# Performance work log

Hardware: AMD Instinct MI355X
Metric: run time of the kernel (lower is better)

Reference implementation:

```python
import jax, jax.numpy as jnp
import numpy as np

B, SC, ST = 16, 512, 512
DP, DC = 256, 128
D = DP + 2 * DC          # 512 = d_model
H, L, DFF = 8, 2, 2048
NCAT, NCONT = 1000, 2048


def sin_embed(vals, d, scale=1000.0):
    # vectorized sinusoidal_time_embedding: even dims -> sin(angle), odd dims -> cos(angle)
    i = jnp.arange(d, dtype=jnp.float32)
    ang = vals.astype(jnp.float32)[..., None] / jnp.power(scale, i / d)
    return jnp.where(i % 2 == 0, jnp.sin(ang), jnp.cos(ang))


def layer_norm(x, g, b, eps=1e-5):
    m = jnp.mean(x, -1, keepdims=True)
    v = jnp.mean(jnp.square(x - m), -1, keepdims=True)
    return (x - m) / jnp.sqrt(v + eps) * g + b


def setup_inputs() -> dict:
    key = jax.random.key(0)
    ks = jax.random.split(key, 16)
    s = 0.02
    def n(k, shape, scale=s):
        return jax.random.normal(k, shape, dtype=jnp.float32) * scale
    return {
        "context_cat": jax.random.randint(ks[0], (B, SC), 0, NCAT),
        "context_time": jax.random.uniform(ks[1], (B, SC), dtype=jnp.float32) * 100.0,
        "context_f0": jax.random.uniform(ks[2], (B, SC), dtype=jnp.float32) * 500.0,
        "target_cat": jax.random.randint(ks[3], (B, ST), 0, NCAT),
        "target_time": jax.random.uniform(ks[4], (B, ST), dtype=jnp.float32) * 100.0,
        "target_f0": jax.random.uniform(ks[5], (B, ST), dtype=jnp.float32) * 500.0,
        "cat_table": n(ks[6], (NCAT, DP), 1.0),
        "cont_table": sin_embed(jnp.arange(NCONT, dtype=jnp.float32), DC),  # frozen sin table
        "pad_emb": n(ks[7], (D,), 1.0),
        "Wq": n(ks[8], (L, D, D)), "bq": jnp.zeros((L, D)),
        "Wk": n(ks[9], (L, D, D)), "bk": jnp.zeros((L, D)),
        "Wv": n(ks[10], (L, D, D)), "bv": jnp.zeros((L, D)),
        "Wo": n(ks[11], (L, D, D)), "bo": jnp.zeros((L, D)),
        "ln1g": jnp.ones((L, D)), "ln1b": jnp.zeros((L, D)),
        "ln2g": jnp.ones((L, D)), "ln2b": jnp.zeros((L, D)),
        "W1": n(ks[12], (L, D, DFF)), "b1": jnp.zeros((L, DFF)),
        "W2": n(ks[13], (L, DFF, D)), "b2": jnp.zeros((L, D)),
    }


def reference(context_cat, context_time, context_f0, target_cat, target_time, target_f0,
              cat_table, cont_table, pad_emb,
              Wq, bq, Wk, bk, Wv, bv, Wo, bo,
              ln1g, ln1b, ln2g, ln2b, W1, b1, W2, b2):
    def embed(cat, tm, f0):
        pad = cat < 0
        e = jnp.concatenate(
            [cat_table[jnp.maximum(cat, 0)], sin_embed(tm, DC), sin_embed(f0, DC)], axis=-1)
        return jnp.where(pad[..., None], pad_emb, e), pad

    ce, cp = embed(context_cat, context_time, context_f0)
    te, tp = embed(target_cat, target_time, target_f0)
    x = jnp.concatenate([ce, te], axis=1)                       # [B, SC+ST, D]
    bias = jnp.where(jnp.concatenate([cp, tp], 1), -1e9, 0.0)[:, None, None, :]
    hd = D // H
    inv_sqrt = 1.0 / np.sqrt(hd).astype(np.float32)

    def step(h, p):
        wq, bq_, wk, bk_, wv, bv_, wo, bo_, g1, c1, g2, c2, w1, d1, w2, d2 = p
        Bn, S, _ = h.shape
        q = (h @ wq + bq_).reshape(Bn, S, H, hd)
        k = (h @ wk + bk_).reshape(Bn, S, H, hd)
        v = (h @ wv + bv_).reshape(Bn, S, H, hd)
        scores = jnp.einsum('bqhd,bkhd->bhqk', q, k) * inv_sqrt + bias
        attn = jax.nn.softmax(scores, axis=-1)
        o = jnp.einsum('bhqk,bkhd->bqhd', attn, v).reshape(Bn, S, D)
        h = layer_norm(h + o @ wo + bo_, g1, c1)                # post-norm (torch default)
        f = jax.nn.relu(h @ w1 + d1) @ w2 + d2
        return layer_norm(h + f, g2, c2), None

    x, _ = jax.lax.scan(step, x, (Wq, bq, Wk, bk, Wv, bv, Wo, bo,
                                  ln1g, ln1b, ln2g, ln2b, W1, b1, W2, b2))
    out = x[:, SC:, :]
    pred_cat = out[..., :DP] @ cat_table.T
    pred_time = out[..., DP:DP + DC] @ cont_table.T
    pred_f0 = out[..., DP + DC:] @ cont_table.T
    return pred_cat, pred_time, pred_f0
```

## Files before the change

### kernel.cpp

```cpp
#include <hip/hip_runtime.h>


typedef _Float16 half8 __attribute__((ext_vector_type(8)));
typedef _Float16 half4 __attribute__((ext_vector_type(4)));
typedef float f32x4 __attribute__((ext_vector_type(4)));

__device__ __forceinline__ void gl2lds16(const _Float16* g, _Float16* l) {
    __builtin_amdgcn_global_load_lds(
        (const __attribute__((address_space(1))) void*)g,
        (__attribute__((address_space(3))) void*)l, 16, 0, 0);
}

__global__ void cast_f32_f16_k(const float* __restrict__ in, _Float16* __restrict__ out,
                               long nsrc, long ntot) {
    long i = (long)blockIdx.x * blockDim.x + threadIdx.x;
    long stride = (long)gridDim.x * blockDim.x;
    for (; i < ntot; i += stride) out[i] = i < nsrc ? (_Float16)in[i] : (_Float16)0.f;
}

__global__ void tcast_k(const float* __restrict__ in, _Float16* __restrict__ out,
                        int R, int C, long zs, int rowoff) {
    __shared__ float tile[32][33];
    long z = blockIdx.z;
    const float* src = in + z * (long)R * C;
    _Float16* dst = out + z * zs + (long)rowoff * R;
    int c0 = blockIdx.x * 32, r0 = blockIdx.y * 32;
    for (int i = threadIdx.y; i < 32; i += 8)
        tile[i][threadIdx.x] = src[(long)(r0 + i) * C + c0 + threadIdx.x];
    __syncthreads();
    for (int i = threadIdx.y; i < 32; i += 8)
        dst[(long)(c0 + i) * R + r0 + threadIdx.x] = (_Float16)tile[threadIdx.x][i];
}

__global__ void bcat_k(const float* __restrict__ bq, const float* __restrict__ bk,
                       const float* __restrict__ bv, float* __restrict__ out, int L) {
    int i = blockIdx.x * 256 + threadIdx.x;
    if (i >= L * 1536) return;
    int l = i / 1536, j = i - l * 1536;
    float v = j < 512 ? bq[l * 512 + j] : (j < 1024 ? bk[l * 512 + j - 512] : bv[l * 512 + j - 1024]);
    out[i] = v;
}

__global__ void vtrans_k(const _Float16* __restrict__ qkv, _Float16* __restrict__ vT) {
    __shared__ _Float16 tile[32][33];
    int bh = blockIdx.z; int b = bh >> 3, h = bh & 7;
    int s0 = blockIdx.x * 32, d0 = blockIdx.y * 32;
    const _Float16* src = qkv + ((long)b * 1024) * 1536 + 1024 + h * 64;
    _Float16* dst = vT + (long)bh * 64 * 1024;
    for (int i = threadIdx.y; i < 32; i += 8)
        tile[i][threadIdx.x] = src[(long)(s0 + i) * 1536 + d0 + threadIdx.x];
    __syncthreads();
    for (int i = threadIdx.y; i < 32; i += 8)
        dst[(long)(d0 + i) * 1024 + s0 + threadIdx.x] = tile[threadIdx.x][i];
}

__global__ __launch_bounds__(128) void embed_k(
    const int* __restrict__ ccat, const float* __restrict__ ctime, const float* __restrict__ cf0,
    const int* __restrict__ tcat, const float* __restrict__ ttime, const float* __restrict__ tf0,
    const float* __restrict__ cat_table, const float* __restrict__ pad_emb,
    float* __restrict__ xf, _Float16* __restrict__ xb, float* __restrict__ biasKey) {
    int t = blockIdx.x;
    int b = t >> 10, s = t & 1023;
    int j = b * 512 + (s & 511);
    int cat; float tm, f0;
    if (s < 512) { cat = ccat[j]; tm = ctime[j]; f0 = cf0[j]; }
    else         { cat = tcat[j]; tm = ttime[j]; f0 = tf0[j]; }
    bool pad = cat < 0;
    if (threadIdx.x == 0) biasKey[t] = pad ? -1e9f : 0.f;
    int c = cat < 0 ? 0 : cat;
    #pragma unroll
    for (int u = 0; u < 4; u++) {
        int d = threadIdx.x * 4 + u;
        float val;
        if (pad) val = pad_emb[d];
        else if (d < 256) val = cat_table[(long)c * 256 + d];
        else {
            float base = (d < 384) ? tm : f0;
            int i = (d < 384) ? (d - 256) : (d - 384);
            float ang = base / powf(1000.f, (float)i * (1.f / 128.f));
            val = (i & 1) ? cosf(ang) : sinf(ang);
        }
        long o = (long)t * 512 + d;
        xf[o] = val;
        xb[o] = (_Float16)val;
    }
}

__global__ __launch_bounds__(256) void layernorm_k(
    float* xf, _Float16* __restrict__ xb,
    const float* __restrict__ g, const float* __restrict__ beta) {
    long row = blockIdx.x;
    int tid = threadIdx.x;
    float* xr = xf + row * 512;
    float v0 = xr[tid], v1 = xr[tid + 256];
    float s = v0 + v1, q = v0 * v0 + v1 * v1;
    #pragma unroll
    for (int o = 32; o; o >>= 1) { s += __shfl_down(s, o); q += __shfl_down(q, o); }
    __shared__ float rs[4], rq[4];
    if ((tid & 63) == 0) { rs[tid >> 6] = s; rq[tid >> 6] = q; }
    __syncthreads();
    s = rs[0] + rs[1] + rs[2] + rs[3];
    q = rq[0] + rq[1] + rq[2] + rq[3];
    float mean = s * (1.f / 512.f);
    float var = q * (1.f / 512.f) - mean * mean;
    float rstd = rsqrtf(var + 1e-5f);
    float y0 = (v0 - mean) * rstd * g[tid] + beta[tid];
    float y1 = (v1 - mean) * rstd * g[tid + 256] + beta[tid + 256];
    xr[tid] = y0; xr[tid + 256] = y1;
    xb[row * 512 + tid] = (_Float16)y0;
    xb[row * 512 + tid + 256] = (_Float16)y1;
}

__global__ __launch_bounds__(256, 3) void flash_k(
    const _Float16* __restrict__ QKV, const _Float16* __restrict__ VT,
    const float* __restrict__ biasKey, _Float16* __restrict__ O) {
    const int S = 1024, D = 512, LDQ = 1536, NT = 16;
    int bh = blockIdx.x; int b = bh >> 3, h = bh & 7;
    int qt = blockIdx.y;
    int tid = threadIdx.x, w = tid >> 6, lane = tid & 63;
    int g = lane >> 4, q15 = lane & 15;

    __shared__ __align__(16) _Float16 Ks[2][64 * 64];
    __shared__ __align__(16) _Float16 VTs[2][64 * 64];
    __shared__ __align__(16) _Float16 Ps[4][16][72];
    __shared__ __align__(16) float biasLds[1024];

    {
        const float* bsrc = biasKey + (long)b * S;
        f32x4 bv4 = *(const f32x4*)&bsrc[tid * 4];
        #pragma unroll
        for (int r = 0; r < 4; r++) bv4[r] *= 1.442695041f;
        *(f32x4*)&biasLds[tid * 4] = bv4;
    }

    int qrow = qt * 64 + w * 16 + q15;
    const _Float16* qp = QKV + ((long)(b * S + qrow)) * LDQ + h * 64 + g * 8;
    half8 qf[2];
    qf[0] = *(const half8*)(qp);
    qf[1] = *(const half8*)(qp + 32);
    const _Float16 qsc = (_Float16)0.1803368801f;
    #pragma unroll
    for (int kk = 0; kk < 2; kk++)
        #pragma unroll
        for (int i = 0; i < 8; i++) qf[kk][i] *= qsc;

    const _Float16* kbase = QKV + 512 + ((long)b * S) * LDQ + h * 64;
    const _Float16* vbase = VT + (long)bh * 64 * S;

    auto stageK = [&](int buf, int kt) {
        #pragma unroll
        for (int i = 0; i < 2; i++) {
            int c = tid + i * 256;
            int row = c >> 3, p = c & 7;
            int s = p ^ (row & 7);
            gl2lds16(kbase + (long)(kt * 64 + row) * LDQ + s * 8, &Ks[buf][c * 8]);
        }
    };
    auto stageV = [&](int buf, int kt) {
        #pragma unroll
        for (int i = 0; i < 2; i++) {
            int c = tid + i * 256;
            int row = c >> 3, p = c & 7;
            int s = p ^ (row & 7);
            gl2lds16(vbase + (long)row * S + kt * 64 + s * 8, &VTs[buf][c * 8]);
        }
    };

    f32x4 acc_o[4];
    #pragma unroll
    for (int i = 0; i < 4; i++)
        #pragma unroll
        for (int r = 0; r < 4; r++) acc_o[i][r] = 0.f;
    float m_run = -1e30f, l_run = 0.f;

    auto QK = [&](int kt, f32x4 (&s)[4]) {
        #pragma unroll
        for (int mf = 0; mf < 4; mf++)
            #pragma unroll
            for (int r = 0; r < 4; r++) s[mf][r] = 0.f;
        int buf = kt & 1;
        __builtin_amdgcn_s_setprio(1);
        #pragma unroll
        for (int kk = 0; kk < 2; kk++)
            #pragma unroll
            for (int mf = 0; mf < 4; mf++) {
                int row = mf * 16 + q15;
                half8 kf = *(const half8*)&Ks[buf][row * 64 + (((kk * 4 + g) ^ (row & 7)) * 8)];
                s[mf] = __builtin_amdgcn_mfma_f32_16x16x32_f16(kf, qf[kk], s[mf], 0, 0, 0);
            }
        __builtin_amdgcn_s_setprio(0);
    };

    auto SMPV = [&](int kt, f32x4 (&s)[4]) {
        float mt = -1e30f;
        #pragma unroll
        for (int mf = 0; mf < 4; mf++) {
            f32x4 b4 = *(const f32x4*)&biasLds[kt * 64 + mf * 16 + g * 4];
            #pragma unroll
            for (int r = 0; r < 4; r++) {
                float sv = s[mf][r] + b4[r];
                s[mf][r] = sv;
                mt = fmaxf(mt, sv);
            }
        }
        mt = fmaxf(mt, __shfl_xor(mt, 16));
        mt = fmaxf(mt, __shfl_xor(mt, 32));

        float rsum = 0.f;
        if (__all(mt - m_run <= 8.f)) {
            #pragma unroll
            for (int mf = 0; mf < 4; mf++)
                #pragma unroll
                for (int r = 0; r < 4; r++) {
                    float p = exp2f(s[mf][r] - m_run);
                    s[mf][r] = p; rsum += p;
                }
        } else {
            float m_new = fmaxf(m_run, mt);
            float scale = exp2f(m_run - m_new);
            #pragma unroll
            for (int mf = 0; mf < 4; mf++)
                #pragma unroll
                for (int r = 0; r < 4; r++) {
                    float p = exp2f(s[mf][r] - m_new);
                    s[mf][r] = p; rsum += p;
                }
            float sc[4];
            #pragma unroll
            for (int r = 0; r < 4; r++) sc[r] = __shfl(scale, g * 4 + r);
            #pragma unroll
            for (int nf = 0; nf < 4; nf++)
                #pragma unroll
                for (int r = 0; r < 4; r++) acc_o[nf][r] *= sc[r];
            l_run *= scale;
            m_run = m_new;
        }
        rsum += __shfl_xor(rsum, 16);
        rsum += __shfl_xor(rsum, 32);
        l_run += rsum;

        #pragma unroll
        for (int mf = 0; mf < 4; mf++) {
            half4 h4;
            #pragma unroll
            for (int r = 0; r < 4; r++) h4[r] = (_Float16)s[mf][r];
            *(half4*)&Ps[w][q15][mf * 16 + g * 4] = h4;
        }

        int buf = kt & 1;
        __builtin_amdgcn_s_setprio(1);
        #pragma unroll
        for (int kk = 0; kk < 2; kk++) {
            half8 pa = *(const half8*)&Ps[w][q15][kk * 32 + g * 8];
            #pragma unroll
            for (int nf = 0; nf < 4; nf++) {
                int row = nf * 16 + q15;
                half8 vf = *(const half8*)&VTs[buf][row * 64 + (((kk * 4 + g) ^ (row & 7)) * 8)];
                acc_o[nf] = __builtin_amdgcn_mfma_f32_16x16x32_f16(pa, vf, acc_o[nf], 0, 0, 0);
            }
        }
        __builtin_amdgcn_s_setprio(0);
    };

    f32x4 sA[4], sB[4];
    stageK(0, 0); stageV(0, 0); stageK(1, 1);
    __syncthreads();
    QK(0, sA);

    for (int t = 0; t < NT; t += 2) {
        __syncthreads();
        if (t + 2 < NT) stageK(t & 1, t + 2);
        if (t + 1 < NT) stageV((t + 1) & 1, t + 1);
        if (t + 1 < NT) QK(t + 1, sB);
        SMPV(t, sA);
        __syncthreads();
        if (t + 3 < NT) stageK((t + 1) & 1, t + 3);
        if (t + 2 < NT) stageV(t & 1, t + 2);
        if (t + 2 < NT) QK(t + 2, sA);
        SMPV(t + 1, sB);
    }

    float linv = 1.f / l_run;
    float lv[4];
    #pragma unroll
    for (int r = 0; r < 4; r++) lv[r] = __shfl(linv, g * 4 + r);
    _Float16* obase = O + ((long)(b * S + qt * 64 + w * 16)) * D + h * 64;
    #pragma unroll
    for (int nf = 0; nf < 4; nf++)
        #pragma unroll
        for (int r = 0; r < 4; r++) {
            int row = g * 4 + r;
            obase[(long)row * D + nf * 16 + q15] = (_Float16)(acc_o[nf][r] * lv[r]);
        }
}

__global__ __launch_bounds__(256) void gemm_nt(
    const _Float16* __restrict__ A, long lda, long sA1, long sA2,
    const _Float16* __restrict__ Bm, long ldb, long sB1, long sB2,
    float* Cf, _Float16* Cb, long ldc, long sC1, long sC2,
    const float* __restrict__ bias, long sb1, long sb2,
    const float* resid,
    int M, int N, int K, int Z2, float alpha, int relu) {
    int z = blockIdx.z;
    int z1 = z / Z2, z2 = z - z1 * Z2;
    A  += z1 * sA1 + z2 * sA2;
    Bm += z1 * sB1 + z2 * sB2;
    long coff = z1 * sC1 + z2 * sC2;
    if (bias) bias += z1 * sb1 + z2 * sb2;

    int gx = gridDim.x;
    int nwg = gx * gridDim.y;
    int bid = blockIdx.y * gx + blockIdx.x;
    int q = nwg >> 3, r = nwg & 7;
    int xcd = bid & 7, ii = bid >> 3;
    int swz = (xcd < r ? xcd * (q + 1) : r * (q + 1) + (xcd - r) * q) + ii;
    int m0 = (swz / gx) * 128;
    int n0 = (swz % gx) * 128;

    __shared__ __align__(16) _Float16 As[3][128 * 32];
    __shared__ __align__(16) _Float16 Bs[3][128 * 32];

    int tid = threadIdx.x;
    int lane = tid & 63;
    int w = tid >> 6;
    int wr = (w >> 1) << 6;
    int wc = (w & 1) << 6;

    f32x4 acc[4][4];
    #pragma unroll
    for (int i = 0; i < 4; i++)
        #pragma unroll
        for (int jj = 0; jj < 4; jj++) { acc[i][jj][0] = 0.f; acc[i][jj][1] = 0.f; acc[i][jj][2] = 0.f; acc[i][jj][3] = 0.f; }

    int fr = lane & 15;
    int g = lane >> 4;
    int rs8 = (g ^ (fr & 3)) * 8;

    auto stage = [&](int buf, int kt) {
        #pragma unroll
        for (int i = 0; i < 2; i++) {
            int idx = tid + i * 256;
            int row = idx >> 2, s = idx & 3;
            int sg = s ^ (row & 3);
            gl2lds16(A + (long)(m0 + row) * lda + kt * 32 + sg * 8, &As[buf][idx * 8]);
            gl2lds16(Bm + (long)(n0 + row) * ldb + kt * 32 + sg * 8, &Bs[buf][idx * 8]);
        }
    };

    int nk = K >> 5;
    stage(0, 0);
    stage(1, 1);

    for (int t = 0; t < nk; ++t) {
        if (t + 1 < nk) asm volatile("s_waitcnt vmcnt(4)" ::: "memory");
        else            asm volatile("s_waitcnt vmcnt(0)" ::: "memory");
        __builtin_amdgcn_s_barrier();
        __builtin_amdgcn_sched_barrier(0);
        int cur = t % 3;
        if (t + 2 < nk) stage((t + 2) % 3, t + 2);

        half8 af[4], bfv[4];
        #pragma unroll
        for (int m = 0; m < 4; m++) af[m] = *(const half8*)&As[cur][(wr + m * 16 + fr) * 32 + rs8];
        #pragma unroll
        for (int n = 0; n < 4; n++) bfv[n] = *(const half8*)&Bs[cur][(wc + n * 16 + fr) * 32 + rs8];
        #pragma unroll
        for (int m = 0; m < 4; m++)
            #pragma unroll
            for (int n = 0; n < 4; n++)
                acc[m][n] = __builtin_amdgcn_mfma_f32_16x16x32_f16(af[m], bfv[n], acc[m][n], 0, 0, 0);
    }

    int fq = lane >> 4;
    #pragma unroll
    for (int m = 0; m < 4; m++) {
        #pragma unroll
        for (int jj = 0; jj < 4; jj++) {
            long row = m0 + wr + m * 16 + fq * 4 + jj;
            #pragma unroll
            for (int n = 0; n < 4; n++) {
                int col = n0 + wc + n * 16 + fr;
                if (col < N) {
                    float v = acc[m][n][jj] * alpha;
                    if (bias) v += bias[col];
                    long o = coff + row * ldc + col;
                    if (resid) v += resid[o];
                    if (relu) v = fmaxf(v, 0.f);
                    if (Cf) Cf[o] = v;
                    if (Cb) Cb[o] = (_Float16)v;
                }
            }
        }
    }
}

extern "C" void kernel_launch(void* const* d_in, const int* in_sizes, int n_in,
                              void* d_out, int out_size, void* d_ws, size_t ws_size,
                              hipStream_t stream) {
    const int Bn = 16, S = 1024, D = 512, H = 8, L = 2, DFF = 2048, NCAT = 1000, NCONT = 2048;
    const long M = (long)Bn * S;

    const int*   ccat      = (const int*)d_in[0];
    const float* ctime     = (const float*)d_in[1];
    const float* cf0       = (const float*)d_in[2];
    const int*   tcat      = (const int*)d_in[3];
    const float* ttime     = (const float*)d_in[4];
    const float* tf0       = (const float*)d_in[5];
    const float* cat_table = (const float*)d_in[6];
    const float* cont_tab  = (const float*)d_in[7];
    const float* pad_emb   = (const float*)d_in[8];
    const float* Wq = (const float*)d_in[9];
    const float* bq = (const float*)d_in[10];
    const float* Wk = (const float*)d_in[11];
    const float* bk = (const float*)d_in[12];
    const float* Wv = (const float*)d_in[13];
    const float* bv = (const float*)d_in[14];
    const float* Wo = (const float*)d_in[15];
    const float* bo = (const float*)d_in[16];
    const float* ln1g = (const float*)d_in[17];
    const float* ln1b = (const float*)d_in[18];
    const float* ln2g = (const float*)d_in[19];
    const float* ln2b = (const float*)d_in[20];
    const float* W1 = (const float*)d_in[21];
    const float* b1 = (const float*)d_in[22];
    const float* W2 = (const float*)d_in[23];
    const float* b2 = (const float*)d_in[24];

    char* wsb = (char*)d_ws;
    size_t off = 0;
    auto alloc = [&](size_t bytes) -> void* {
        off = (off + 255) & ~(size_t)255;
        void* p = wsb + off; off += bytes; return p;
    };

    float*     xf      = (float*)alloc(M * D * 4);
    _Float16*  xb      = (_Float16*)alloc(M * D * 2);
    _Float16*  qkv     = (_Float16*)alloc(M * 3 * D * 2);
    _Float16*  vT      = (_Float16*)alloc(M * D * 2);
    _Float16*  ob      = (_Float16*)alloc(M * D * 2);
    float*     biasKey = (float*)alloc(M * 4);
    _Float16*  WqkvT = (_Float16*)alloc((size_t)L * 3 * D * D * 2);
    float*     bqkv  = (float*)alloc((size_t)L * 3 * D * 4);
    _Float16*  WoT  = (_Float16*)alloc((size_t)L * D * D * 2);
    _Float16*  W1T  = (_Float16*)alloc((size_t)L * D * DFF * 2);
    _Float16*  W2T  = (_Float16*)alloc((size_t)L * DFF * D * 2);
    _Float16*  catT = (_Float16*)alloc((size_t)1024 * 256 * 2);
    _Float16*  conT = (_Float16*)alloc((size_t)NCONT * 128 * 2);

    size_t need_ffh = (size_t)M * DFF * 2;
    _Float16* ffh;
    size_t offAl = (off + 255) & ~(size_t)255;
    if (offAl + need_ffh <= ws_size) ffh = (_Float16*)alloc(need_ffh);
    else ffh = (_Float16*)d_out;

    auto gemm = [&](const _Float16* A, long lda, long sA1, long sA2,
                    const _Float16* Bm, long ldb, long sB1, long sB2,
                    float* Cf, _Float16* Cb, long ldc, long sC1, long sC2,
                    const float* bias, long sb1, long sb2,
                    const float* resid, int Mm, int Nn, int Kk,
                    int Z1, int Z2, float alpha, int relu) {
        dim3 gdim((Nn + 127) / 128, (Mm + 127) / 128, Z1 * Z2);
        gemm_nt<<<gdim, 256, 0, stream>>>(A, lda, sA1, sA2, Bm, ldb, sB1, sB2,
                                          Cf, Cb, ldc, sC1, sC2, bias, sb1, sb2,
                                          resid, Mm, Nn, Kk, Z2, alpha, relu);
    };

    dim3 tb(32, 8);
    tcast_k<<<dim3(D / 32, D / 32, L), tb, 0, stream>>>(Wq, WqkvT, D, D, (long)3 * D * D, 0);
    tcast_k<<<dim3(D / 32, D / 32, L), tb, 0, stream>>>(Wk, WqkvT, D, D, (long)3 * D * D, D);
    tcast_k<<<dim3(D / 32, D / 32, L), tb, 0, stream>>>(Wv, WqkvT, D, D, (long)3 * D * D, 2 * D);
    bcat_k<<<dim3((L * 1536 + 255) / 256), 256, 0, stream>>>(bq, bk, bv, bqkv, L);
    tcast_k<<<dim3(D / 32, D / 32, L), tb, 0, stream>>>(Wo, WoT, D, D, (long)D * D, 0);
    tcast_k<<<dim3(DFF / 32, D / 32, L), tb, 0, stream>>>(W1, W1T, D, DFF, (long)D * DFF, 0);
    tcast_k<<<dim3(D / 32, DFF / 32, L), tb, 0, stream>>>(W2, W2T, DFF, D, (long)DFF * D, 0);
    cast_f32_f16_k<<<dim3(512), 256, 0, stream>>>(cat_table, catT, (long)NCAT * 256, (long)1024 * 256);
    cast_f32_f16_k<<<dim3(512), 256, 0, stream>>>(cont_tab, conT, (long)NCONT * 128, (long)NCONT * 128);

    embed_k<<<dim3((unsigned)M), 128, 0, stream>>>(ccat, ctime, cf0, tcat, ttime, tf0,
                                                   cat_table, pad_emb, xf, xb, biasKey);

    for (int l = 0; l < L; l++) {
        gemm(xb, D, 0, 0, WqkvT + (size_t)l * 3 * D * D, D, 0, 0, nullptr, qkv, 3 * D, 0, 0,
             bqkv + (size_t)l * 3 * D, 0, 0, nullptr, (int)M, 3 * D, D, 1, 1, 1.f, 0);
        vtrans_k<<<dim3(32, 2, Bn * H), tb, 0, stream>>>(qkv, vT);

        flash_k<<<dim3(Bn * H, S / 64), 256, 0, stream>>>(qkv, vT, biasKey, ob);

        gemm(ob, D, 0, 0, WoT + (size_t)l * D * D, D, 0, 0, xf, nullptr, D, 0, 0,
             bo + l * D, 0, 0, xf, (int)M, D, D, 1, 1, 1.f, 0);
        layernorm_k<<<dim3((unsigned)M), 256, 0, stream>>>(xf, xb, ln1g + l * D, ln1b + l * D);

        gemm(xb, D, 0, 0, W1T + (size_t)l * D * DFF, D, 0, 0, nullptr, ffh, DFF, 0, 0,
             b1 + l * DFF, 0, 0, nullptr, (int)M, DFF, D, 1, 1, 1.f, 1);
        gemm(ffh, DFF, 0, 0, W2T + (size_t)l * DFF * D, DFF, 0, 0, xf, nullptr, D, 0, 0,
             b2 + l * D, 0, 0, xf, (int)M, D, DFF, 1, 1, 1.f, 0);
        layernorm_k<<<dim3((unsigned)M), 256, 0, stream>>>(xf, xb, ln2g + l * D, ln2b + l * D);
    }

    float* out_cat  = (float*)d_out;
    float* out_time = out_cat + (size_t)Bn * 512 * NCAT;
    float* out_f0   = out_time + (size_t)Bn * 512 * NCONT;
    gemm(xb + (size_t)512 * D, D, (long)S * D, 0,
         catT, 256, 0, 0,
         out_cat, nullptr, NCAT, (long)512 * NCAT, 0,
         nullptr, 0, 0, nullptr, 512, NCAT, 256, Bn, 1, 1.f, 0);
    gemm(xb + (size_t)512 * D + 256, D, (long)S * D, 0,
         conT, 128, 0, 0,
         out_time, nullptr, NCONT, (long)512 * NCONT, 0,
         nullptr, 0, 0, nullptr, 512, NCONT, 128, Bn, 1, 1.f, 0);
    gemm(xb + (size_t)512 * D + 384, D, (long)S * D, 0,
         conT, 128, 0, 0,
         out_f0, nullptr, NCONT, (long)512 * NCONT, 0,
         nullptr, 0, 0, nullptr, 512, NCONT, 128, Bn, 1, 1.f, 0);
}
```

Baseline: 935.0 us.

## Widen flash blocks to 128 queries, shuffle P in registers, double-buffer GEMM

The flash attention kernel now runs 512 threads per block covering 128 query rows, so each K/V tile staged into LDS is shared by twice as many waves. The P tile no longer goes through an LDS round trip: it is converted with cvt_pkrtz and moved into MFMA operand layout using permlane32_swap and ds_swizzle. The GEMM goes from triple to double buffering with launch bounds of 5 blocks, cutting LDS per block to fit more blocks per CU. In exchange the GEMM has less prefetch depth and an extra barrier per k-step, and round-toward-zero conversion slightly changes the P rounding.

```diff
diff --git a/kernel.cpp b/kernel.cpp
--- a/kernel.cpp
+++ b/kernel.cpp
@@ -4,6 +4,8 @@
 typedef _Float16 half8 __attribute__((ext_vector_type(8)));
 typedef _Float16 half4 __attribute__((ext_vector_type(4)));
 typedef float f32x4 __attribute__((ext_vector_type(4)));
+typedef unsigned int uint2v __attribute__((ext_vector_type(2)));
+typedef unsigned int uint4v __attribute__((ext_vector_type(4)));
 
 __device__ __forceinline__ void gl2lds16(const _Float16* g, _Float16* l) {
     __builtin_amdgcn_global_load_lds(
@@ -111,7 +113,7 @@
     xb[row * 512 + tid + 256] = (_Float16)y1;
 }
 
-__global__ __launch_bounds__(256, 3) void flash_k(
+__global__ __launch_bounds__(512, 4) void flash_k(
     const _Float16* __restrict__ QKV, const _Float16* __restrict__ VT,
     const float* __restrict__ biasKey, _Float16* __restrict__ O) {
     const int S = 1024, D = 512, LDQ = 1536, NT = 16;
@@ -122,18 +124,15 @@
 
     __shared__ __align__(16) _Float16 Ks[2][64 * 64];
     __shared__ __align__(16) _Float16 VTs[2][64 * 64];
-    __shared__ __align__(16) _Float16 Ps[4][16][72];
     __shared__ __align__(16) float biasLds[1024];
 
     {
         const float* bsrc = biasKey + (long)b * S;
-        f32x4 bv4 = *(const f32x4*)&bsrc[tid * 4];
-        #pragma unroll
-        for (int r = 0; r < 4; r++) bv4[r] *= 1.442695041f;
-        *(f32x4*)&biasLds[tid * 4] = bv4;
+        biasLds[tid]       = bsrc[tid] * 1.442695041f;
+        biasLds[tid + 512] = bsrc[tid + 512] * 1.442695041f;
     }
 
-    int qrow = qt * 64 + w * 16 + q15;
+    int qrow = qt * 128 + w * 16 + q15;
     const _Float16* qp = QKV + ((long)(b * S + qrow)) * LDQ + h * 64 + g * 8;
     half8 qf[2];
     qf[0] = *(const half8*)(qp);
@@ -148,22 +147,14 @@
     const _Float16* vbase = VT + (long)bh * 64 * S;
 
     auto stageK = [&](int buf, int kt) {
-        #pragma unroll
-        for (int i = 0; i < 2; i++) {
-            int c = tid + i * 256;
-            int row = c >> 3, p = c & 7;
-            int s = p ^ (row & 7);
-            gl2lds16(kbase + (long)(kt * 64 + row) * LDQ + s * 8, &Ks[buf][c * 8]);
-        }
+        int row = tid >> 3, p = tid & 7;
+        int s = p ^ (row & 7);
+        gl2lds16(kbase + (long)(kt * 64 + row) * LDQ + s * 8, &Ks[buf][tid * 8]);
     };
     auto stageV = [&](int buf, int kt) {
-        #pragma unroll
-        for (int i = 0; i < 2; i++) {
-            int c = tid + i * 256;
-            int row = c >> 3, p = c & 7;
-            int s = p ^ (row & 7);
-            gl2lds16(vbase + (long)row * S + kt * 64 + s * 8, &VTs[buf][c * 8]);
-        }
+        int row = tid >> 3, p = tid & 7;
+        int s = p ^ (row & 7);
+        gl2lds16(vbase + (long)row * S + kt * 64 + s * 8, &VTs[buf][tid * 8]);
     };
 
     f32x4 acc_o[4];
@@ -172,6 +163,7 @@
         #pragma unroll
         for (int r = 0; r < 4; r++) acc_o[i][r] = 0.f;
     float m_run = -1e30f, l_run = 0.f;
+    bool gOdd = (g & 1) != 0;
 
     auto QK = [&](int kt, f32x4 (&s)[4]) {
         #pragma unroll
@@ -239,27 +231,42 @@
         rsum += __shfl_xor(rsum, 32);
         l_run += rsum;
 
+        unsigned pk[4][2];
         #pragma unroll
         for (int mf = 0; mf < 4; mf++) {
-            half4 h4;
-            #pragma unroll
-            for (int r = 0; r < 4; r++) h4[r] = (_Float16)s[mf][r];
-            *(half4*)&Ps[w][q15][mf * 16 + g * 4] = h4;
+            auto h0 = __builtin_amdgcn_cvt_pkrtz(s[mf][0], s[mf][1]);
+            auto h1 = __builtin_amdgcn_cvt_pkrtz(s[mf][2], s[mf][3]);
+            pk[mf][0] = __builtin_bit_cast(unsigned, h0);
+            pk[mf][1] = __builtin_bit_cast(unsigned, h1);
         }
 
         int buf = kt & 1;
-        __builtin_amdgcn_s_setprio(1);
         #pragma unroll
         for (int kk = 0; kk < 2; kk++) {
-            half8 pa = *(const half8*)&Ps[w][q15][kk * 32 + g * 8];
+            unsigned wA[2], wB[2];
+            #pragma unroll
+            for (int wi = 0; wi < 2; wi++) {
+                uint2v r2 = __builtin_amdgcn_permlane32_swap(
+                    pk[2 * kk][wi], pk[2 * kk + 1][wi], false, false);
+                unsigned na = r2[0];
+                unsigned nb = r2[1];
+                unsigned sa = (unsigned)__builtin_amdgcn_ds_swizzle((int)na, 0x401F);
+                unsigned sb = (unsigned)__builtin_amdgcn_ds_swizzle((int)nb, 0x401F);
+                wA[wi] = gOdd ? sb : na;
+                wB[wi] = gOdd ? nb : sa;
+            }
+            uint4v paw;
+            paw[0] = wA[0]; paw[1] = wA[1]; paw[2] = wB[0]; paw[3] = wB[1];
+            half8 pa = __builtin_bit_cast(half8, paw);
+            __builtin_amdgcn_s_setprio(1);
             #pragma unroll
             for (int nf = 0; nf < 4; nf++) {
                 int row = nf * 16 + q15;
                 half8 vf = *(const half8*)&VTs[buf][row * 64 + (((kk * 4 + g) ^ (row & 7)) * 8)];
                 acc_o[nf] = __builtin_amdgcn_mfma_f32_16x16x32_f16(pa, vf, acc_o[nf], 0, 0, 0);
             }
-        }
-        __builtin_amdgcn_s_setprio(0);
+            __builtin_amdgcn_s_setprio(0);
+        }
     };
 
     f32x4 sA[4], sB[4];
@@ -284,7 +291,7 @@
     float lv[4];
     #pragma unroll
     for (int r = 0; r < 4; r++) lv[r] = __shfl(linv, g * 4 + r);
-    _Float16* obase = O + ((long)(b * S + qt * 64 + w * 16)) * D + h * 64;
+    _Float16* obase = O + ((long)(b * S + qt * 128 + w * 16)) * D + h * 64;
     #pragma unroll
     for (int nf = 0; nf < 4; nf++)
         #pragma unroll
@@ -294,7 +301,7 @@
         }
 }
 
-__global__ __launch_bounds__(256) void gemm_nt(
+__global__ __launch_bounds__(256, 5) void gemm_nt(
     const _Float16* __restrict__ A, long lda, long sA1, long sA2,
     const _Float16* __restrict__ Bm, long ldb, long sB1, long sB2,
     float* Cf, _Float16* Cb, long ldc, long sC1, long sC2,
@@ -317,8 +324,8 @@
     int m0 = (swz / gx) * 128;
     int n0 = (swz % gx) * 128;
 
-    __shared__ __align__(16) _Float16 As[3][128 * 32];
-    __shared__ __align__(16) _Float16 Bs[3][128 * 32];
+    __shared__ __align__(16) _Float16 As[2][128 * 32];
+    __shared__ __align__(16) _Float16 Bs[2][128 * 32];
 
     int tid = threadIdx.x;
     int lane = tid & 63;
@@ -349,16 +356,19 @@
 
     int nk = K >> 5;
     stage(0, 0);
-    stage(1, 1);
 
     for (int t = 0; t < nk; ++t) {
-        if (t + 1 < nk) asm volatile("s_waitcnt vmcnt(4)" ::: "memory");
-        else            asm volatile("s_waitcnt vmcnt(0)" ::: "memory");
+        __builtin_amdgcn_s_barrier();
+        if (t + 1 < nk) {
+            stage((t + 1) & 1, t + 1);
+            asm volatile("s_waitcnt vmcnt(4)" ::: "memory");
+        } else {
+            asm volatile("s_waitcnt vmcnt(0)" ::: "memory");
+        }
         __builtin_amdgcn_s_barrier();
         __builtin_amdgcn_sched_barrier(0);
-        int cur = t % 3;
-        if (t + 2 < nk) stage((t + 2) % 3, t + 2);
-
+
+        int cur = t & 1;
         half8 af[4], bfv[4];
         #pragma unroll
         for (int m = 0; m < 4; m++) af[m] = *(const half8*)&As[cur][(wr + m * 16 + fr) * 32 + rs8];
@@ -484,7 +494,7 @@
              bqkv + (size_t)l * 3 * D, 0, 0, nullptr, (int)M, 3 * D, D, 1, 1, 1.f, 0);
         vtrans_k<<<dim3(32, 2, Bn * H), tb, 0, stream>>>(qkv, vT);
 
-        flash_k<<<dim3(Bn * H, S / 64), 256, 0, stream>>>(qkv, vT, biasKey, ob);
+        flash_k<<<dim3(Bn * H, S / 128), 512, 0, stream>>>(qkv, vT, biasKey, ob);
 
         gemm(ob, D, 0, 0, WoT + (size_t)l * D * D, D, 0, 0, xf, nullptr, D, 0, 0,
              bo + l * D, 0, 0, xf, (int)M, D, D, 1, 1, 1.f, 0);
```

Result: no change. 936.6 us (median of 5 runs) (+0.2%).
